# Kernel tuning notes

Measured on AMD Instinct MI355X. Metric: run time of the kernel, lower is better.

## Reference

```python
import jax, jax.numpy as jnp
import numpy as np
import math

B, S, D = 2, 2048, 1024
E = 1024          # dim_embedds
H = 16            # num_heads
DK = E // H       # d_k = 64


def _xavier(key, shape):
    fan_out, fan_in = shape
    limit = math.sqrt(6.0 / (fan_in + fan_out))
    return jax.random.uniform(key, shape, jnp.float32, -limit, limit)


def setup_inputs() -> dict:
    key = jax.random.key(0)
    k_x, k_qkv, k_o = jax.random.split(key, 3)
    return {
        "x": jax.random.normal(k_x, (B, S, D), jnp.float32),
        "W_qkv": _xavier(k_qkv, (3 * E, D)),   # torch Linear weight [out, in]
        "b_qkv": jnp.zeros((3 * E,), jnp.float32),
        "W_o": _xavier(k_o, (E, E)),
        "b_o": jnp.zeros((E,), jnp.float32),
    }


def reference(x, W_qkv, b_qkv, W_o, b_o):
    b, s, _ = x.shape
    # fused QKV projection: [B,S,3E] -> [B,S,H,3,DK] (per-head interleaved q,k,v)
    qkv = (jnp.einsum("bsd,ed->bse", x, W_qkv) + b_qkv).reshape(b, s, H, 3, DK)
    qkv = jnp.transpose(qkv, (3, 0, 2, 1, 4))  # [3,B,H,S,DK]
    q, k, v = qkv[0], qkv[1], qkv[2]
    scores = jnp.einsum("bhqd,bhkd->bhqk", q, k) / math.sqrt(DK)  # [B,H,S,S]
    attn = jax.nn.softmax(scores, axis=-1)
    out = jnp.einsum("bhqk,bhkd->bhqd", attn, v)  # [B,H,S,DK]
    out = jnp.transpose(out, (0, 2, 1, 3)).reshape(b, s, E)  # combine heads
    return jnp.einsum("bse,fe->bsf", out, W_o) + b_o
```

## Files before the change

kernel.cpp:

```cpp
#include <hip/hip_runtime.h>
#include <stdint.h>


typedef unsigned short u16;
typedef unsigned int u32;
typedef __attribute__((ext_vector_type(8))) short bf16x8;
typedef __attribute__((ext_vector_type(4))) float f32x4;
typedef __attribute__((ext_vector_type(4))) unsigned int u32x4;
typedef __attribute__((ext_vector_type(4))) unsigned short u16x4;
typedef __attribute__((ext_vector_type(2))) unsigned int u32x2;

#define LOG2E 1.44269504088896340736f
#define NSHIFT -17.312340490667562f
#define QSCALE 0.18033688011112057f

#if __has_builtin(__builtin_amdgcn_exp2f)
#define EXP2(x) __builtin_amdgcn_exp2f(x)
#else
#define EXP2(x) exp2f(x)
#endif

static __device__ __forceinline__ float bf2f(u16 u) {
  union { u32 u; float f; } v; v.u = ((u32)u) << 16; return v.f;
}
static __device__ __forceinline__ u16 f2bf(float f) {
  union { float f; u32 u; } v; v.f = f;
  return (u16)((v.u + 0x7FFFu + ((v.u >> 16) & 1u)) >> 16);
}
static __device__ __forceinline__ u32 pack2bf(u32 lo, u32 hi) {
  return __builtin_amdgcn_perm(hi, lo, 0x07060302u);
}

static __device__ __forceinline__ bool sniff_f32(const u16* __restrict__ x) {
  const int lane = threadIdx.x & 63;
  const u16 v = x[lane * 2];
  const int e = (v >> 7) & 0xFF;
  const unsigned long long m = __ballot(e >= 100 && e <= 140);
  return __popcll(m) < 48;
}

static __device__ __forceinline__ void async16(const u16* g, u16* l) {
  __builtin_amdgcn_global_load_lds((const __attribute__((address_space(1))) void*)g,
                                   (__attribute__((address_space(3))) void*)l, 16, 0, 0);
}

static __device__ __forceinline__ bf16x8 ld8cv(const void* p, size_t e, bool isf32) {
  bf16x8 r;
  if (isf32) {
    const u32x4 a = *(const u32x4*)((const float*)p + e);
    const u32x4 b = *(const u32x4*)((const float*)p + e + 4);
    u32* rr = (u32*)&r;
    rr[0] = pack2bf(a[0] + 0x8000u, a[1] + 0x8000u);
    rr[1] = pack2bf(a[2] + 0x8000u, a[3] + 0x8000u);
    rr[2] = pack2bf(b[0] + 0x8000u, b[1] + 0x8000u);
    rr[3] = pack2bf(b[2] + 0x8000u, b[3] + 0x8000u);
  } else {
    r = *(const bf16x8*)((const u16*)p + e);
  }
  return r;
}
static __device__ __forceinline__ float ldscalar(const void* p, int i, bool isf32) {
  return isf32 ? ((const float*)p)[i] : bf2f(((const u16*)p)[i]);
}

__global__ void convert_all(const void* __restrict__ x,  const void* __restrict__ wq,
                            const void* __restrict__ bq, const void* __restrict__ wo,
                            const void* __restrict__ bo,
                            u16* __restrict__ xd, u16* __restrict__ wqd,
                            u16* __restrict__ bqd, u16* __restrict__ wod,
                            u16* __restrict__ bod) {
  const bool f32in = sniff_f32((const u16*)x);
  const int b = blockIdx.x;
  const void* src; u16* dst; size_t base; int seg = 0;
  if (b < 4096)      { src = x;  dst = xd;  base = (size_t)b * 256; }
  else if (b < 7168) { src = wq; dst = wqd; base = (size_t)(b - 4096) * 256; seg = 1; }
  else if (b < 7171) { src = bq; dst = bqd; base = (size_t)(b - 7168) * 256; seg = 2; }
  else if (b < 8195) { src = wo; dst = wod; base = (size_t)(b - 7171) * 256; }
  else               { src = bo; dst = bod; base = 0; }
  const size_t i = base + threadIdx.x;
  float scale = 1.f;
  if (seg == 1) { const u32 row = (u32)(i >> 8); if (row % 192u < 64u) scale = QSCALE; }
  else if (seg == 2) { if (((u32)(i * 4)) % 192u < 64u) scale = QSCALE; }
  if (f32in) {
    const f32x4 a = ((const f32x4*)src)[i];
    u32 pb[4];
#pragma unroll
    for (int j = 0; j < 4; ++j) pb[j] = __float_as_uint(a[j] * scale) + 0x8000u;
    u32x2 o; o[0] = pack2bf(pb[0], pb[1]); o[1] = pack2bf(pb[2], pb[3]);
    ((u32x2*)dst)[i] = o;
  } else {
    u16x4 v = ((const u16x4*)src)[i];
    if (scale != 1.f) {
#pragma unroll
      for (int j = 0; j < 4; ++j) v[j] = f2bf(bf2f(v[j]) * scale);
    }
    ((u16x4*)dst)[i] = v;
  }
}

template <int MODE, bool BPRE, int TM>
__global__ __launch_bounds__(256, 3) void gemm_nt(
    const u16* __restrict__ A, const void* __restrict__ Bw,
    const void* __restrict__ bias, int K, int N,
    void* __restrict__ out0, u16* __restrict__ out1, u16* __restrict__ out2,
    const u16* __restrict__ xsniff)
{
  constexpr int MI = TM / 32;
  __shared__ __align__(16) u16 smem[TM * 32 + 4096];
  u16* As = smem;
  u16* Bs = smem + TM * 32;

  const bool f32in = sniff_f32(xsniff);
  const bool bw32  = BPRE ? false : f32in;

  const int tid  = threadIdx.x;
  const int wave = tid >> 6, lane = tid & 63;
  const int wm = wave >> 1, wn = wave & 1;
  const int fr = lane & 15, fq = lane >> 4;
  const int m0 = blockIdx.x * TM, n0 = blockIdx.y * 128;

  const int arows = TM / 4;
  const u16* gA0 = A + (size_t)(m0 + wave * arows + (lane >> 2)) * K + (lane & 3) * 8;
  const u16* gA1 = gA0 + (size_t)16 * K;
  u16* lA = As + wave * (arows * 32);

  const u16* gB0 = (const u16*)Bw + (size_t)(n0 + wave * 32 + (lane >> 2)) * K + (lane & 3) * 8;
  const u16* gB1 = gB0 + (size_t)16 * K;
  u16* lB = Bs + wave * 1024;

  const int srow = tid >> 2, scol = (tid & 3) * 8;
  const int li   = srow * 32 + scol;
  const size_t eB = (size_t)(n0 + srow) * K + scol;
  const size_t half = (size_t)64 * K;

  f32x4 acc[MI][4];
#pragma unroll
  for (int i = 0; i < MI; ++i)
#pragma unroll
    for (int j = 0; j < 4; ++j) acc[i][j] = (f32x4){0.f, 0.f, 0.f, 0.f};

  for (int kt = 0; kt < K; kt += 32) {
    if (BPRE) {
      __syncthreads();
      async16(gA0, lA);
      if (TM == 128) async16(gA1, lA + 512);
      async16(gB0, lB);
      async16(gB1, lB + 512);
      gA0 += 32; gA1 += 32; gB0 += 32; gB1 += 32;
      __syncthreads();
    } else {
      const bf16x8 b0 = ld8cv(Bw, eB + kt,        bw32);
      const bf16x8 b1 = ld8cv(Bw, eB + half + kt, bw32);
      __syncthreads();
      async16(gA0, lA);
      if (TM == 128) async16(gA1, lA + 512);
      gA0 += 32; gA1 += 32;
      *(bf16x8*)(Bs + li)        = b0;
      *(bf16x8*)(Bs + li + 2048) = b1;
      __syncthreads();
    }

    bf16x8 af[MI], bfv[4];
#pragma unroll
    for (int mi = 0; mi < MI; ++mi)
      af[mi] = *(const bf16x8*)(As + (wm * (TM / 2) + mi * 16 + fr) * 32 + fq * 8);
#pragma unroll
    for (int ni = 0; ni < 4; ++ni)
      bfv[ni] = *(const bf16x8*)(Bs + (wn * 64 + ni * 16 + fr) * 32 + fq * 8);
#pragma unroll
    for (int mi = 0; mi < MI; ++mi)
#pragma unroll
      for (int ni = 0; ni < 4; ++ni)
        acc[mi][ni] = __builtin_amdgcn_mfma_f32_16x16x32_bf16(af[mi], bfv[ni], acc[mi][ni], 0, 0, 0);
  }

  if (MODE == 0) {
    __syncthreads();
    u16* swT = smem + wave * 1152;
    const int region = blockIdx.y * 2 + wn;
    const int h = region / 3, which = region % 3;
    float bvv[4];
#pragma unroll
    for (int ni = 0; ni < 4; ++ni)
      bvv[ni] = ldscalar(bias, region * 64 + ni * 16 + fr, bw32);
    const float qs = BPRE ? 1.f : QSCALE;

    if (which < 2) {
      u16* outp = (which == 0) ? (u16*)out0 : out1;
      const float sc = (which == 0) ? qs : 1.f;
#pragma unroll
      for (int mi = 0; mi < MI; ++mi) {
#pragma unroll
        for (int ni = 0; ni < 4; ++ni)
#pragma unroll
          for (int r = 0; r < 4; ++r)
            swT[(fq * 4 + r) * 72 + ni * 16 + fr] = f2bf((acc[mi][ni][r] + bvv[ni]) * sc);
#pragma unroll
        for (int u = 0; u < 2; ++u) {
          const int idx = u * 64 + lane;
          const int m_l = idx >> 3, dkc = idx & 7;
          const bf16x8 row = *(const bf16x8*)(swT + m_l * 72 + dkc * 8);
          const int m = m0 + wm * (TM / 2) + mi * 16 + m_l;
          const int bb = m >> 11, s = m & 2047;
          *(bf16x8*)(outp + ((size_t)(bb * 16 + h) * 2048 + s) * 64 + dkc * 8) = row;
        }
      }
    } else {
#pragma unroll
      for (int ni = 0; ni < 4; ++ni) {
#pragma unroll
        for (int mi = 0; mi < MI; ++mi) {
          u16x4 pk;
#pragma unroll
          for (int r = 0; r < 4; ++r) pk[r] = f2bf(acc[mi][ni][r] + bvv[ni]);
          *(u16x4*)(swT + fr * 72 + mi * 16 + fq * 4) = pk;
        }
#pragma unroll
        for (int u = 0; u < 2; ++u) {
          const int idx = u * 64 + lane;
          const int dk_l = idx >> 3, mc = idx & 7;
          const bf16x8 row = *(const bf16x8*)(swT + dk_l * 72 + mc * 8);
          const int mb = m0 + wm * (TM / 2) + mc * 8;
          const int bb = mb >> 11, s0 = mb & 2047;
          *(bf16x8*)(out2 + ((size_t)((bb * 16 + h) * 64 + ni * 16 + dk_l)) * 2048 + s0) = row;
        }
      }
    }
  } else {
#pragma unroll
    for (int ni = 0; ni < 4; ++ni) {
      const int e = n0 + wn * 64 + ni * 16 + fr;
      const float bv = ldscalar(bias, e, bw32);
#pragma unroll
      for (int mi = 0; mi < MI; ++mi) {
#pragma unroll
        for (int r = 0; r < 4; ++r) {
          const int m = m0 + wm * (TM / 2) + mi * 16 + fq * 4 + r;
          const float v = acc[mi][ni][r] + bv;
          if (f32in) ((float*)out0)[(size_t)m * N + e] = v;
          else       ((u16*)out0)[(size_t)m * N + e]   = f2bf(v);
        }
      }
    }
  }
}

__global__ __launch_bounds__(256, 2) void flash_attn(
    const u16* __restrict__ Q, const u16* __restrict__ Kk,
    const u16* __restrict__ Vt, u16* __restrict__ AO)
{
  __shared__ __align__(16) u16 Kt[2][64 * 64];
  __shared__ __align__(16) u16 Vl[2][64 * 64];
  __shared__ __align__(16) u16 Plt[4 * 32 * 64];

  const int tid  = threadIdx.x;
  const int wave = tid >> 6, lane = tid & 63;
  const int fr = lane & 15, fq = lane >> 4;
  const int sw = fr & 7;
  const int bh = blockIdx.y;
  const int q0 = blockIdx.x * 128;
  const size_t base = (size_t)bh * 2048 * 64;

  bf16x8 ones;
#pragma unroll
  for (int j = 0; j < 8; ++j) ones[j] = (short)0x3F80;

  bf16x8 qf[2][2];
#pragma unroll
  for (int qq = 0; qq < 2; ++qq) {
    const u16* qrow = Q + base + (size_t)(q0 + wave * 32 + qq * 16 + fr) * 64 + fq * 8;
    qf[qq][0] = *(const bf16x8*)(qrow);
    qf[qq][1] = *(const bf16x8*)(qrow + 32);
  }

  f32x4 oacc[2][4];
#pragma unroll
  for (int qq = 0; qq < 2; ++qq)
#pragma unroll
    for (int i = 0; i < 4; ++i) oacc[qq][i] = (f32x4){0.f, 0.f, 0.f, 0.f};
  f32x4 lD[2] = {(f32x4){0.f, 0.f, 0.f, 0.f}, (f32x4){0.f, 0.f, 0.f, 0.f}};

  const int srow = tid >> 3, sc = tid & 7;
  const int so = srow * 64 + (sc ^ (srow & 7)) * 8;
  const u16* gK = Kk + base + (size_t)srow * 64 + sc * 8;
  const u16* gV = Vt + base + (size_t)srow * 2048 + sc * 8;
  u16* pw = Plt + wave * 32 * 64;

  bf16x8 k0 = *(const bf16x8*)(gK);
  bf16x8 k1 = *(const bf16x8*)(gK + 32 * 64);
  bf16x8 v0 = *(const bf16x8*)(gV);
  bf16x8 v1 = *(const bf16x8*)(gV + 32 * 2048);

  for (int kt = 0; kt < 32; ++kt) {
    u16* KtW = Kt[kt & 1];
    u16* VlW = Vl[kt & 1];
    *(bf16x8*)(KtW + so)           = k0;
    *(bf16x8*)(KtW + so + 32 * 64) = k1;
    *(bf16x8*)(VlW + so)           = v0;
    *(bf16x8*)(VlW + so + 32 * 64) = v1;

    gK += 64 * 64;
    gV += 64;
    k0 = *(const bf16x8*)(gK);
    k1 = *(const bf16x8*)(gK + 32 * 64);
    v0 = *(const bf16x8*)(gV);
    v1 = *(const bf16x8*)(gV + 32 * 2048);

    __syncthreads();

    f32x4 sacc[2][4];
#pragma unroll
    for (int qq = 0; qq < 2; ++qq)
#pragma unroll
      for (int cb = 0; cb < 4; ++cb)
        sacc[qq][cb] = (f32x4){NSHIFT, NSHIFT, NSHIFT, NSHIFT};
#pragma unroll
    for (int cb = 0; cb < 4; ++cb) {
      const u16* kr = KtW + (cb * 16 + fr) * 64;
      const int c0 = (fq ^ sw) * 8;
      bf16x8 kf0 = *(const bf16x8*)(kr + c0);
      bf16x8 kf1 = *(const bf16x8*)(kr + (c0 ^ 32));
#pragma unroll
      for (int qq = 0; qq < 2; ++qq) {
        sacc[qq][cb] = __builtin_amdgcn_mfma_f32_16x16x32_bf16(kf0, qf[qq][0], sacc[qq][cb], 0, 0, 0);
        sacc[qq][cb] = __builtin_amdgcn_mfma_f32_16x16x32_bf16(kf1, qf[qq][1], sacc[qq][cb], 0, 0, 0);
      }
    }

#pragma unroll
    for (int qq = 0; qq < 2; ++qq) {
      const int prow = (qq * 16 + fr) * 64;
#pragma unroll
      for (int cb = 0; cb < 4; ++cb) {
        u32 pb[4];
#pragma unroll
        for (int r = 0; r < 4; ++r)
          pb[r] = __float_as_uint(EXP2(sacc[qq][cb][r])) + 0x8000u;
        u32x2 pk;
        pk[0] = pack2bf(pb[0], pb[1]);
        pk[1] = pack2bf(pb[2], pb[3]);
        const int ch = ((2 * cb + (fq >> 1)) ^ sw) * 8 + (fq & 1) * 4;
        *(u32x2*)(pw + prow + ch) = pk;
      }
    }

#pragma unroll
    for (int g = 0; g < 2; ++g) {
      const int pc = ((4 * g + fq) ^ sw) * 8;
      bf16x8 pf0 = *(const bf16x8*)(pw + fr * 64 + pc);
      bf16x8 pf1 = *(const bf16x8*)(pw + (16 + fr) * 64 + pc);
#pragma unroll
      for (int db = 0; db < 4; ++db) {
        bf16x8 vf = *(const bf16x8*)(VlW + (db * 16 + fr) * 64 + pc);
        oacc[0][db] = __builtin_amdgcn_mfma_f32_16x16x32_bf16(vf, pf0, oacc[0][db], 0, 0, 0);
        oacc[1][db] = __builtin_amdgcn_mfma_f32_16x16x32_bf16(vf, pf1, oacc[1][db], 0, 0, 0);
      }
      lD[0] = __builtin_amdgcn_mfma_f32_16x16x32_bf16(ones, pf0, lD[0], 0, 0, 0);
      lD[1] = __builtin_amdgcn_mfma_f32_16x16x32_bf16(ones, pf1, lD[1], 0, 0, 0);
    }
  }

  const int b = bh >> 4, h = bh & 15;
#pragma unroll
  for (int qq = 0; qq < 2; ++qq) {
    const float inv = 1.0f / lD[qq][0];
    const int s = q0 + wave * 32 + qq * 16 + fr;
    u16* orow = AO + ((size_t)(b * 2048 + s)) * 1024 + h * 64;
#pragma unroll
    for (int db = 0; db < 4; ++db) {
      u16x4 ov;
#pragma unroll
      for (int r = 0; r < 4; ++r) ov[r] = f2bf(oacc[qq][db][r] * inv);
      *(u16x4*)(orow + db * 16 + fq * 4) = ov;
    }
  }
}

extern "C" void kernel_launch(void* const* d_in, const int* in_sizes, int n_in,
                              void* d_out, int out_size, void* d_ws, size_t ws_size,
                              hipStream_t stream) {
  const void* x    = d_in[0];
  const void* Wqkv = d_in[1];
  const void* bqkv = d_in[2];
  const void* Wo   = d_in[3];
  const void* bo   = d_in[4];
  const u16* xs    = (const u16*)x;

  const size_t HEADS = 32, S = 2048, DK = 64;
  const size_t NQ = HEADS * S * DK;
  u16* Qs = (u16*)d_ws;
  u16* Ks = Qs + NQ;
  u16* Vt = Ks + NQ;
  u16* XA = Vt + NQ;

  u16* Wqb = XA + 2 * S * 1024;
  u16* Wob = Wqb + 3145728;
  u16* bqb = Wob + 1048576;
  u16* bob = bqb + 3072;
  const size_t need_big = ((size_t)(bob + 1024) - (size_t)d_ws);
  const bool big = ws_size >= need_big;

  if (big) {
    convert_all<<<8196, 256, 0, stream>>>(x, Wqkv, bqkv, Wo, bo,
                                          XA, Wqb, bqb, Wob, bob);
    gemm_nt<0, true, 128><<<dim3(32, 24), 256, 0, stream>>>(XA, Wqb, bqb, 1024, 3072,
                                                            Qs, Ks, Vt, xs);
    flash_attn<<<dim3(16, 32), 256, 0, stream>>>(Qs, Ks, Vt, XA);
    gemm_nt<1, true, 64><<<dim3(64, 8), 256, 0, stream>>>(XA, Wob, bob, 1024, 1024,
                                                          d_out, nullptr, nullptr, xs);
  } else {
    convert_all<<<4096, 256, 0, stream>>>(x, Wqkv, bqkv, Wo, bo,
                                          XA, XA, XA, XA, XA);
    gemm_nt<0, false, 128><<<dim3(32, 24), 256, 0, stream>>>(XA, Wqkv, bqkv, 1024, 3072,
                                                             Qs, Ks, Vt, xs);
    flash_attn<<<dim3(16, 32), 256, 0, stream>>>(Qs, Ks, Vt, XA);
    gemm_nt<1, false, 64><<<dim3(64, 8), 256, 0, stream>>>(XA, Wo, bo, 1024, 1024,
                                                           d_out, nullptr, nullptr, xs);
  }
}
```

Baseline: 183.6 us.

## Double-buffer GEMM LDS tiles with register prefetch of next K-slice

Replaces the global_load_lds async copies and the two barriers per K step with a register-staged, double-buffered LDS scheme. Each iteration writes the prefetched tile into one of two LDS buffers, issues global loads for the next K slice, then takes a single barrier before the MFMA work. The goal is to hide global load latency behind compute and cut synchronisation. In exchange it doubles LDS use, which may lower occupancy under launch_bounds(256,3), and it adds register pressure. The last iteration also issues a wasted reload of slice zero.

```diff
diff --git a/kernel.cpp b/kernel.cpp
--- a/kernel.cpp
+++ b/kernel.cpp
@@ -37,11 +37,6 @@
   const int e = (v >> 7) & 0xFF;
   const unsigned long long m = __ballot(e >= 100 && e <= 140);
   return __popcll(m) < 48;
-}
-
-static __device__ __forceinline__ void async16(const u16* g, u16* l) {
-  __builtin_amdgcn_global_load_lds((const __attribute__((address_space(1))) void*)g,
-                                   (__attribute__((address_space(3))) void*)l, 16, 0, 0);
 }
 
 static __device__ __forceinline__ bf16x8 ld8cv(const void* p, size_t e, bool isf32) {
@@ -106,9 +101,8 @@
     const u16* __restrict__ xsniff)
 {
   constexpr int MI = TM / 32;
-  __shared__ __align__(16) u16 smem[TM * 32 + 4096];
-  u16* As = smem;
-  u16* Bs = smem + TM * 32;
+  constexpr int TILE = TM * 32;
+  __shared__ __align__(16) u16 smem[2][TILE + 4096];
 
   const bool f32in = sniff_f32(xsniff);
   const bool bw32  = BPRE ? false : f32in;
@@ -119,17 +113,9 @@
   const int fr = lane & 15, fq = lane >> 4;
   const int m0 = blockIdx.x * TM, n0 = blockIdx.y * 128;
 
-  const int arows = TM / 4;
-  const u16* gA0 = A + (size_t)(m0 + wave * arows + (lane >> 2)) * K + (lane & 3) * 8;
-  const u16* gA1 = gA0 + (size_t)16 * K;
-  u16* lA = As + wave * (arows * 32);
-
-  const u16* gB0 = (const u16*)Bw + (size_t)(n0 + wave * 32 + (lane >> 2)) * K + (lane & 3) * 8;
-  const u16* gB1 = gB0 + (size_t)16 * K;
-  u16* lB = Bs + wave * 1024;
-
   const int srow = tid >> 2, scol = (tid & 3) * 8;
   const int li   = srow * 32 + scol;
+  const size_t eA = (size_t)(m0 + srow) * K + scol;
   const size_t eB = (size_t)(n0 + srow) * K + scol;
   const size_t half = (size_t)64 * K;
 
@@ -139,26 +125,27 @@
 #pragma unroll
     for (int j = 0; j < 4; ++j) acc[i][j] = (f32x4){0.f, 0.f, 0.f, 0.f};
 
+  bf16x8 a0 = *(const bf16x8*)(A + eA);
+  bf16x8 a1;
+  if (TM == 128) a1 = *(const bf16x8*)(A + eA + half);
+  bf16x8 b0 = ld8cv(Bw, eB, bw32);
+  bf16x8 b1 = ld8cv(Bw, eB + half, bw32);
+
   for (int kt = 0; kt < K; kt += 32) {
-    if (BPRE) {
-      __syncthreads();
-      async16(gA0, lA);
-      if (TM == 128) async16(gA1, lA + 512);
-      async16(gB0, lB);
-      async16(gB1, lB + 512);
-      gA0 += 32; gA1 += 32; gB0 += 32; gB1 += 32;
-      __syncthreads();
-    } else {
-      const bf16x8 b0 = ld8cv(Bw, eB + kt,        bw32);
-      const bf16x8 b1 = ld8cv(Bw, eB + half + kt, bw32);
-      __syncthreads();
-      async16(gA0, lA);
-      if (TM == 128) async16(gA1, lA + 512);
-      gA0 += 32; gA1 += 32;
-      *(bf16x8*)(Bs + li)        = b0;
-      *(bf16x8*)(Bs + li + 2048) = b1;
-      __syncthreads();
-    }
+    u16* As = smem[(kt >> 5) & 1];
+    u16* Bs = As + TILE;
+    *(bf16x8*)(As + li) = a0;
+    if (TM == 128) *(bf16x8*)(As + li + 2048) = a1;
+    *(bf16x8*)(Bs + li) = b0;
+    *(bf16x8*)(Bs + li + 2048) = b1;
+
+    const int ktn = (kt + 32 < K) ? kt + 32 : 0;
+    a0 = *(const bf16x8*)(A + eA + ktn);
+    if (TM == 128) a1 = *(const bf16x8*)(A + eA + half + ktn);
+    b0 = ld8cv(Bw, eB + ktn, bw32);
+    b1 = ld8cv(Bw, eB + half + ktn, bw32);
+
+    __syncthreads();
 
     bf16x8 af[MI], bfv[4];
 #pragma unroll
@@ -176,7 +163,7 @@
 
   if (MODE == 0) {
     __syncthreads();
-    u16* swT = smem + wave * 1152;
+    u16* swT = smem[0] + wave * 1152;
     const int region = blockIdx.y * 2 + wn;
     const int h = region / 3, which = region % 3;
     float bvv[4];
```

New measurement: 186.4 us. About the same (+1.6%).
